# Optimization experiments

Hardware: AMD Instinct MI355X
Metric: run time of the kernel (lower is better)

Reference implementation:

```python
import jax, jax.numpy as jnp
import numpy as np

B, N, DIM, H, DH = 2, 1024, 1024, 8, 64
DI = H * DH  # 512
K = 4        # depthwise conv kernel
EPS = 1.1920929e-07  # float32 eps (torch RMSNorm default)


def setup_inputs() -> dict:
    key = jax.random.key(0)
    ks = jax.random.split(key, 12)
    s = lambda k, shape, sc=0.02: jax.random.normal(k, shape, jnp.float32) * sc
    return dict(
        x=jax.random.normal(ks[0], (B, N, DIM), jnp.float32),
        w_rms=jnp.ones((DIM,), jnp.float32),
        wq=s(ks[1], (DIM, DI)), wk=s(ks[2], (DIM, DI)), wv=s(ks[3], (DIM, DI)),
        wo=s(ks[4], (DI, DIM)),
        conv_q=s(ks[5], (DIM, K), 0.3), conv_k=s(ks[6], (DIM, K), 0.3), conv_v=s(ks[7], (DIM, K), 0.3),
        gamma_q=jnp.ones((H, 1, DH), jnp.float32), gamma_k=jnp.ones((H, 1, DH), jnp.float32),
        lr_w=s(ks[8], (DIM, H)), lr_b=jnp.full((H,), -4.0, jnp.float32),
        decay_w=s(ks[9], (DIM, H)), decay_b=jnp.full((H,), 4.0, jnp.float32),
        mom_w=s(ks[10], (DIM, H)), mom_b=jnp.full((H,), 2.0, jnp.float32),
    )


def rmsnorm(x, w):
    return x * jax.lax.rsqrt(jnp.mean(x * x, -1, keepdims=True) + EPS) * w


def mh_rmsnorm(x, gamma):  # x: (b, h, n, d)
    rms = jnp.sqrt(jnp.sum(x * x, -1, keepdims=True)) * (DH ** -0.5)
    return x / jnp.maximum(rms, 1e-8) * gamma


def dwconv(x, w):  # x: (b, n, dim), w: (dim, K) depthwise, padding K//2 -> length n+1
    y = jax.lax.conv_general_dilated(
        x.transpose(0, 2, 1), w[:, None, :], (1,), [(K // 2, K // 2)],
        feature_group_count=DIM, dimension_numbers=('NCW', 'OIW', 'NCW'))
    return y.transpose(0, 2, 1)


def gated_scan(a, x):  # h_t = a_t h_{t-1} + x_t, h_{-1}=0; a:(bh,t), x:(bh,t,d,d)
    def combine(c1, c2):
        a1, x1 = c1
        a2, x2 = c2
        return a1 * a2, a2 * x1 + x2
    _, h = jax.lax.associative_scan(combine, (a[..., None, None], x), axis=1)
    return h


def reference(x, w_rms, wq, wk, wv, wo, conv_q, conv_k, conv_v,
              gamma_q, gamma_k, lr_w, lr_b, decay_w, decay_b, mom_w, mom_b):
    b, n, _ = x.shape
    xa = rmsnorm(x, w_rms)
    qi, ki, vi = dwconv(xa, conv_q), dwconv(xa, conv_k), dwconv(xa, conv_v)
    split = lambda t: t.reshape(b, -1, H, DH).transpose(0, 2, 1, 3)[:, :, :n]  # (b,h,n,d)
    q = mh_rmsnorm(split(qi @ wq), gamma_q)
    k = mh_rmsnorm(split(ki @ wk), gamma_k)
    v = split(vi @ wv)
    fq = q.reshape(b * H, n, DH)
    fk = k.reshape(b * H, n, DH)
    fv = v.reshape(b * H, n, DH)
    sig = jax.nn.sigmoid
    lr = sig(xa @ lr_w + lr_b).transpose(0, 2, 1).reshape(b * H, n)
    decay = sig(xa @ decay_w + decay_b).transpose(0, 2, 1).reshape(b * H, n)
    mom = sig(xa @ mom_w + mom_b).transpose(0, 2, 1).reshape(b * H, n)
    # S_ref = S0 = 0 (fresh state) => pred = 0, delta_vec = -v
    g = jnp.einsum('bti,btj->btij', -fv, fk)          # (bh, n, d, d)
    Z = gated_scan(mom, g)                             # momentum scan
    S = gated_scan(decay, -lr[..., None, None] * Z)    # memory scan
    S_prev = jnp.concatenate([jnp.zeros_like(S[:, :1]), S[:, :-1]], axis=1)
    y = jnp.einsum('btdp,btp->btd', S_prev, fq)        # retrieval y_t = S_{t-1} psi_t
    y = y.reshape(b, H, n, DH).transpose(0, 2, 1, 3).reshape(b, n, DI)
    return y @ wo
```

## Files before the change

### kernel.cpp

```cpp
#include <hip/hip_runtime.h>
#include <math.h>

#define DEV __device__ __forceinline__

constexpr int Bb   = 2;
constexpr int Seq  = 1024;
constexpr int Dim  = 1024;
constexpr int Hh   = 8;
constexpr int Dh   = 64;
constexpr int Di   = 512;
constexpr int BN   = Bb * Seq;
constexpr int NSEQ = Bb * Hh;
constexpr int CHUNK = 32;
constexpr int CLEN  = Seq / CHUNK;
constexpr float EPSV = 1.1920929e-07f;
constexpr int NT   = 16;

typedef _Float16 half8 __attribute__((ext_vector_type(8)));
typedef float    f32x4 __attribute__((ext_vector_type(4)));

DEV float bf2f(unsigned short u) {
  union { unsigned int i; float f; } x; x.i = ((unsigned int)u) << 16; return x.f;
}
DEV unsigned short f2bf(float f) {
  union { float f; unsigned int i; } x; x.f = f;
  unsigned int r = x.i + 0x7fffu + ((x.i >> 16) & 1u);
  return (unsigned short)(r >> 16);
}
DEV float ldin(const void* p, int f32, size_t i) {
  if (f32) return ((const float*)p)[i];
  return bf2f(((const unsigned short*)p)[i]);
}

struct InPtrs { const void* p[17]; int n[17]; };

__global__ __launch_bounds__(64) void k_sniff(InPtrs ip, int* __restrict__ flags) {
  int b = blockIdx.x, tid = threadIdx.x;
  const unsigned short* u = (const unsigned short*)ip.p[b];
  int count = ip.n[b];
  int j = 2 * tid;
  int valid = 0, bad = 0;
  if (j < count) {
    valid = 1;
    float v = bf2f(u[j]);
    float a = fabsf(v);
    if (!(a >= 1e-12f && a <= 1e4f)) bad = 1;
  }
#pragma unroll
  for (int m = 1; m < 64; m <<= 1) { valid += __shfl_xor(valid, m); bad += __shfl_xor(bad, m); }
  if (tid == 0) flags[b] = (2 * bad > valid) ? 1 : 0;
}

__global__ __launch_bounds__(256) void k_prep_w(
    const void* __restrict__ wq, const void* __restrict__ wk,
    const void* __restrict__ wv, const void* __restrict__ wo,
    const int* __restrict__ flags,
    _Float16* __restrict__ wqT, _Float16* __restrict__ wkT,
    _Float16* __restrict__ wvT, _Float16* __restrict__ woT)
{
  int z = blockIdx.z;
  const void* src = (z == 0) ? wq : ((z == 1) ? wk : ((z == 2) ? wv : wo));
  _Float16* dst   = (z == 0) ? wqT : ((z == 1) ? wkT : ((z == 2) ? wvT : woT));
  int f = flags[(z == 0) ? 2 : ((z == 1) ? 3 : ((z == 2) ? 4 : 5))];
  int Kd = (z < 3) ? Dim : Di;
  int Nn = (z < 3) ? Di : Dim;
  int n0 = blockIdx.x * 64, k0 = blockIdx.y * 64;
  if (n0 >= Nn || k0 >= Kd) return;

  __shared__ float tile[64][65];
  int tid = threadIdx.x;
  int r = tid >> 4, c4 = (tid & 15) * 4;
#pragma unroll
  for (int rr = 0; rr < 4; ++rr) {
    int k = rr * 16 + r;
#pragma unroll
    for (int j = 0; j < 4; ++j)
      tile[k][c4 + j] = ldin(src, f, (size_t)(k0 + k) * Nn + n0 + c4 + j);
  }
  __syncthreads();
#pragma unroll
  for (int rr = 0; rr < 4; ++rr) {
    int n = rr * 16 + r;
    _Float16 o4[4];
#pragma unroll
    for (int j = 0; j < 4; ++j) o4[j] = (_Float16)tile[c4 + j][n];
    *(ushort4*)&dst[(size_t)(n0 + n) * Kd + k0 + c4] = *(ushort4*)o4;
  }
}

__global__ __launch_bounds__(256) void k_prep_gamma(
    const void* __restrict__ gq, const void* __restrict__ gk,
    const void* __restrict__ lr_b, const void* __restrict__ decay_b,
    const void* __restrict__ mom_b,
    const int* __restrict__ flags,
    float* __restrict__ gqf, float* __restrict__ gkf, float* __restrict__ gbf)
{
  int tid = threadIdx.x;
  int f9 = flags[9], f10 = flags[10];
  for (int i = tid; i < Di; i += 256) {
    gqf[i] = ldin(gq, f9, i);
    gkf[i] = ldin(gk, f10, i);
  }
  if (tid < 24) {
    int g = tid >> 3, h = tid & 7;
    const void* Bp = (g == 0) ? lr_b : ((g == 1) ? decay_b : mom_b);
    int fB = (g == 0) ? flags[12] : ((g == 1) ? flags[14] : flags[16]);
    gbf[tid] = ldin(Bp, fB, h);
  }
}

__global__ __launch_bounds__(256) void k_prep_gates(
    const void* __restrict__ lr_w, const void* __restrict__ decay_w,
    const void* __restrict__ mom_w, const int* __restrict__ flags,
    _Float16* __restrict__ WgT)
{
  int row = blockIdx.x;
  int tid = threadIdx.x;
  if (row < 24) {
    int g = row >> 3, h = row & 7;
    const void* W = (g == 0) ? lr_w : ((g == 1) ? decay_w : mom_w);
    int f = (g == 0) ? flags[11] : ((g == 1) ? flags[13] : flags[15]);
#pragma unroll
    for (int it = 0; it < 4; ++it) {
      int d = it * 256 + tid;
      WgT[(size_t)row * Dim + d] = (_Float16)ldin(W, f, (size_t)d * Hh + h);
    }
  } else {
#pragma unroll
    for (int it = 0; it < 4; ++it)
      WgT[(size_t)row * Dim + it * 256 + tid] = (_Float16)0.f;
  }
}

__global__ __launch_bounds__(256) void k_prep_conv(
    const void* __restrict__ cq, const void* __restrict__ ck,
    const void* __restrict__ cv, const int* __restrict__ flags,
    _Float16* __restrict__ wcq, _Float16* __restrict__ wck,
    _Float16* __restrict__ wcv)
{
  int tid = blockIdx.x * 256 + threadIdx.x;
  int f6 = flags[6], f7 = flags[7], f8 = flags[8];
  wcq[tid] = (_Float16)ldin(cq, f6, tid);
  wck[tid] = (_Float16)ldin(ck, f7, tid);
  wcv[tid] = (_Float16)ldin(cv, f8, tid);
}

__global__ __launch_bounds__(256) void k_rms(
    const void* __restrict__ x, const void* __restrict__ w_rms,
    const int* __restrict__ flags, _Float16* __restrict__ xaf)
{
  __shared__ float red[4];
  int r = blockIdx.x;
  int tid = threadIdx.x, lane = tid & 63, wid = tid >> 6;
  int fx = flags[0], fw = flags[1];

  size_t rb = (size_t)r * Dim + tid * 4;
  float v0, v1, v2, v3;
  if (fx) {
    float4 u = *(const float4*)((const float*)x + rb);
    v0 = u.x; v1 = u.y; v2 = u.z; v3 = u.w;
  } else {
    ushort4 u = *(const ushort4*)((const unsigned short*)x + rb);
    v0 = bf2f(u.x); v1 = bf2f(u.y); v2 = bf2f(u.z); v3 = bf2f(u.w);
  }
  float ss = v0 * v0 + v1 * v1 + v2 * v2 + v3 * v3;
#pragma unroll
  for (int m = 1; m < 64; m <<= 1) ss += __shfl_xor(ss, m);
  if (lane == 0) red[wid] = ss;
  __syncthreads();
  float scale = rsqrtf((red[0] + red[1] + red[2] + red[3]) * (1.0f / Dim) + EPSV);

  float w0, w1, w2, w3;
  if (fw) {
    float4 u = *(const float4*)((const float*)w_rms + tid * 4);
    w0 = u.x; w1 = u.y; w2 = u.z; w3 = u.w;
  } else {
    ushort4 u = *(const ushort4*)((const unsigned short*)w_rms + tid * 4);
    w0 = bf2f(u.x); w1 = bf2f(u.y); w2 = bf2f(u.z); w3 = bf2f(u.w);
  }
  _Float16 t4[4] = {(_Float16)(v0 * scale * w0), (_Float16)(v1 * scale * w1),
                    (_Float16)(v2 * scale * w2), (_Float16)(v3 * scale * w3)};
  *(ushort4*)&xaf[rb] = *(ushort4*)t4;
}

__global__ __launch_bounds__(256) void k_gates(
    const _Float16* __restrict__ xaf, const _Float16* __restrict__ WgT,
    const float* __restrict__ gbf,
    float* __restrict__ lr, float* __restrict__ decay, float* __restrict__ mom)
{
  __shared__ __align__(16) _Float16 As[64][40];
  __shared__ __align__(16) _Float16 Bs[64][40];

  int tid = threadIdx.x, lane = tid & 63, wvid = tid >> 6;
  int m0 = blockIdx.x * 64;
  int srow = tid >> 2, scol = (tid & 3) * 8;
  int mrow = lane & 15, quad = lane >> 4;

  f32x4 acc[4];
#pragma unroll
  for (int mi = 0; mi < 4; ++mi) acc[mi] = (f32x4){0.f, 0.f, 0.f, 0.f};

  for (int kt = 0; kt < Dim; kt += 32) {
    __syncthreads();
    *(uint4*)&As[srow][scol] = *(const uint4*)&xaf[(size_t)(m0 + srow) * Dim + kt + scol];
    *(uint4*)&Bs[srow][scol] = *(const uint4*)&WgT[(size_t)srow * Dim + kt + scol];
    __syncthreads();
    half8 bfr = *(const half8*)&Bs[wvid * 16 + mrow][quad * 8];
#pragma unroll
    for (int mi = 0; mi < 4; ++mi) {
      half8 afr = *(const half8*)&As[mi * 16 + mrow][quad * 8];
      acc[mi] = __builtin_amdgcn_mfma_f32_16x16x32_f16(afr, bfr, acc[mi], 0, 0, 0);
    }
  }

  int col = wvid * 16 + mrow;
  if (col < 24) {
    int g = col >> 3, h = col & 7;
    float bias = gbf[col];
    float* Op = (g == 0) ? lr : ((g == 1) ? decay : mom);
#pragma unroll
    for (int mi = 0; mi < 4; ++mi) {
#pragma unroll
      for (int r2 = 0; r2 < 4; ++r2) {
        int row = m0 + mi * 16 + quad * 4 + r2;
        int b = row >> 10, t = row & (Seq - 1);
        float z = acc[mi][r2] + bias;
        Op[(b * Hh + h) * Seq + t] = 1.f / (1.f + expf(-z));
      }
    }
  }
}

__global__ __launch_bounds__(256) void k_conv(
    const _Float16* __restrict__ xaf,
    const _Float16* __restrict__ wcq, const _Float16* __restrict__ wck,
    const _Float16* __restrict__ wcv,
    _Float16* __restrict__ qc, _Float16* __restrict__ kc,
    _Float16* __restrict__ vc)
{
  int tb = blockIdx.x, b = blockIdx.y;
  int t0 = tb * NT;
  int c0 = threadIdx.x * 4;

  _Float16 lwq[16], lwk[16], lwv[16];
  *(uint4*)&lwq[0] = *(const uint4*)&wcq[c0 * 4];
  *(uint4*)&lwq[8] = *(const uint4*)&wcq[c0 * 4 + 8];
  *(uint4*)&lwk[0] = *(const uint4*)&wck[c0 * 4];
  *(uint4*)&lwk[8] = *(const uint4*)&wck[c0 * 4 + 8];
  *(uint4*)&lwv[0] = *(const uint4*)&wcv[c0 * 4];
  *(uint4*)&lwv[8] = *(const uint4*)&wcv[c0 * 4 + 8];

  float win[4][4];
  auto loadrow = [&](int ts, float dst[4]) {
    if (ts >= 0 && ts < Seq) {
      ushort4 u = *(const ushort4*)&xaf[((size_t)(b * Seq + ts)) * Dim + c0];
      _Float16 hx[4]; *(ushort4*)hx = u;
      dst[0] = (float)hx[0]; dst[1] = (float)hx[1];
      dst[2] = (float)hx[2]; dst[3] = (float)hx[3];
    } else {
      dst[0] = 0.f; dst[1] = 0.f; dst[2] = 0.f; dst[3] = 0.f;
    }
  };
  loadrow(t0 - 2, win[0]);
  loadrow(t0 - 1, win[1]);
  loadrow(t0,     win[2]);

#pragma unroll
  for (int tt = 0; tt < NT; ++tt) {
    int t = t0 + tt;
    loadrow(t + 1, win[(tt + 3) & 3]);
    const float* r0 = win[(tt + 0) & 3];
    const float* r1 = win[(tt + 1) & 3];
    const float* r2 = win[(tt + 2) & 3];
    const float* r3 = win[(tt + 3) & 3];

    _Float16 tq[4], tk[4], tv[4];
#pragma unroll
    for (int j = 0; j < 4; ++j) {
      float aq = r0[j] * (float)lwq[j * 4 + 0] + r1[j] * (float)lwq[j * 4 + 1]
               + r2[j] * (float)lwq[j * 4 + 2] + r3[j] * (float)lwq[j * 4 + 3];
      float ak = r0[j] * (float)lwk[j * 4 + 0] + r1[j] * (float)lwk[j * 4 + 1]
               + r2[j] * (float)lwk[j * 4 + 2] + r3[j] * (float)lwk[j * 4 + 3];
      float av = r0[j] * (float)lwv[j * 4 + 0] + r1[j] * (float)lwv[j * 4 + 1]
               + r2[j] * (float)lwv[j * 4 + 2] + r3[j] * (float)lwv[j * 4 + 3];
      tq[j] = (_Float16)aq; tk[j] = (_Float16)ak; tv[j] = (_Float16)av;
    }
    size_t o = ((size_t)(b * Seq + t)) * Dim + c0;
    *(ushort4*)&qc[o] = *(ushort4*)tq;
    *(ushort4*)&kc[o] = *(ushort4*)tk;
    *(ushort4*)&vc[o] = *(ushort4*)tv;
  }
}

__global__ __launch_bounds__(256) void k_gemm_bt(
    const _Float16* __restrict__ A0, const _Float16* __restrict__ A1,
    const _Float16* __restrict__ A2,
    const _Float16* __restrict__ B0, const _Float16* __restrict__ B1,
    const _Float16* __restrict__ B2,
    void* __restrict__ C0, void* __restrict__ C1, void* __restrict__ C2,
    const int* __restrict__ flags,
    int Nn, int Kd, int is_final)
{
  int z = blockIdx.z;
  const _Float16* A  = (z == 0) ? A0 : ((z == 1) ? A1 : A2);
  const _Float16* Bt = (z == 0) ? B0 : ((z == 1) ? B1 : B2);
  void* C = (z == 0) ? C0 : ((z == 1) ? C1 : C2);

  __shared__ __align__(16) _Float16 As[64][40];
  __shared__ __align__(16) _Float16 Bs[64][40];

  int tid = threadIdx.x, lane = tid & 63, wvid = tid >> 6;
  int n0 = blockIdx.x * 64, m0 = blockIdx.y * 64;
  int srow = tid >> 2, scol = (tid & 3) * 8;
  int mrow = lane & 15, quad = lane >> 4;

  f32x4 acc[4];
#pragma unroll
  for (int mi = 0; mi < 4; ++mi) acc[mi] = (f32x4){0.f, 0.f, 0.f, 0.f};

  for (int kt = 0; kt < Kd; kt += 32) {
    __syncthreads();
    *(uint4*)&As[srow][scol] = *(const uint4*)&A[(size_t)(m0 + srow) * Kd + kt + scol];
    *(uint4*)&Bs[srow][scol] = *(const uint4*)&Bt[(size_t)(n0 + srow) * Kd + kt + scol];
    __syncthreads();
    half8 bfr = *(const half8*)&Bs[wvid * 16 + mrow][quad * 8];
#pragma unroll
    for (int mi = 0; mi < 4; ++mi) {
      half8 afr = *(const half8*)&As[mi * 16 + mrow][quad * 8];
      acc[mi] = __builtin_amdgcn_mfma_f32_16x16x32_f16(afr, bfr, acc[mi], 0, 0, 0);
    }
  }

  int any_bf16 = 0;
  if (is_final) {
#pragma unroll
    for (int i2 = 0; i2 < 17; ++i2) any_bf16 |= (flags[i2] == 0);
  }

  int col = n0 + wvid * 16 + mrow;
#pragma unroll
  for (int mi = 0; mi < 4; ++mi) {
#pragma unroll
    for (int r2 = 0; r2 < 4; ++r2) {
      int row = m0 + mi * 16 + quad * 4 + r2;
      float v = acc[mi][r2];
      size_t idx = (size_t)row * Nn + col;
      if (!is_final)        ((_Float16*)C)[idx] = (_Float16)v;
      else if (any_bf16)    ((unsigned short*)C)[idx] = f2bf(v);
      else                  ((float*)C)[idx] = v;
    }
  }
}

__global__ __launch_bounds__(256) void k_phaseA(
    const _Float16* __restrict__ kpre, const _Float16* __restrict__ vpre,
    const float* __restrict__ gkf,
    const float* __restrict__ lr, const float* __restrict__ decay,
    const float* __restrict__ mom,
    _Float16* __restrict__ ZS_Z, _Float16* __restrict__ ZS_S,
    float* __restrict__ Mc, float* __restrict__ Dc, float* __restrict__ Wc)
{
  int c = blockIdx.x, s = blockIdx.y;
  int b = s >> 3, h = s & 7;
  int tid = threadIdx.x, lane = tid & 63, wv = tid >> 6;
  int i = tid >> 2, j0 = (tid & 3) * 16;
  __shared__ float kn[CLEN][64], vv[CLEN][64];
  __shared__ float gl[CLEN], gd[CLEN], gm[CLEN];

  {
    int t = tid >> 3, col = (tid & 7) * 8;
    size_t g = ((size_t)(b * Seq + c * CLEN + t)) * Di + h * 64 + col;
    half8 kv = *(const half8*)&kpre[g];
    half8 vvv = *(const half8*)&vpre[g];
#pragma unroll
    for (int j = 0; j < 8; ++j) { kn[t][col + j] = (float)kv[j]; vv[t][col + j] = (float)vvv[j]; }
    if (tid < 96) {
      int which = tid >> 5, t2 = tid & 31;
      const float* gp = (which == 0) ? lr : ((which == 1) ? decay : mom);
      float val = gp[s * Seq + c * CLEN + t2];
      if (which == 0) gl[t2] = val; else if (which == 1) gd[t2] = val; else gm[t2] = val;
    }
  }
  __syncthreads();
  {
    float gk = gkf[h * 64 + lane];
#pragma unroll
    for (int tt = 0; tt < 8; ++tt) {
      int t = wv * 8 + tt;
      float kvv = kn[t][lane];
      float ss = kvv * kvv;
#pragma unroll
      for (int m = 1; m < 64; m <<= 1) ss += __shfl_xor(ss, m);
      kn[t][lane] = kvv * (1.f / fmaxf(sqrtf(ss) * 0.125f, 1e-8f)) * gk;
    }
  }
  __syncthreads();

  float Zl[16], Sl[16];
#pragma unroll
  for (int jj = 0; jj < 16; ++jj) { Zl[jj] = 0.f; Sl[jj] = 0.f; }
  float Mcum = 1.f, Dcum = 1.f, wacc = 0.f;

  for (int t = 0; t < CLEN; ++t) {
    float l = gl[t], dd = gd[t], mm = gm[t];
    float vi = vv[t][i];
    Mcum *= mm;
#pragma unroll
    for (int jj = 0; jj < 16; ++jj) {
      Zl[jj] = fmaf(mm, Zl[jj], -vi * kn[t][j0 + jj]);
      Sl[jj] = fmaf(dd, Sl[jj], -l * Zl[jj]);
    }
    wacc = fmaf(dd, wacc, -l * Mcum);
    Dcum *= dd;
  }
  size_t base = ((size_t)(s * CHUNK + c)) * 4096 + (size_t)i * 64 + j0;
  half8 zo0, zo1, so0, so1;
#pragma unroll
  for (int jj = 0; jj < 8; ++jj) {
    zo0[jj] = (_Float16)Zl[jj];     zo1[jj] = (_Float16)Zl[jj + 8];
    so0[jj] = (_Float16)Sl[jj];     so1[jj] = (_Float16)Sl[jj + 8];
  }
  *(half8*)&ZS_Z[base] = zo0; *(half8*)&ZS_Z[base + 8] = zo1;
  *(half8*)&ZS_S[base] = so0; *(half8*)&ZS_S[base + 8] = so1;
  if (tid == 0) {
    Mc[s * CHUNK + c] = Mcum; Dc[s * CHUNK + c] = Dcum; Wc[s * CHUNK + c] = wacc;
  }
}

__global__ __launch_bounds__(256) void k_phaseB(
    _Float16* __restrict__ ZS_Z, _Float16* __restrict__ ZS_S,
    const float* __restrict__ Mc, const float* __restrict__ Dc,
    const float* __restrict__ Wc)
{
  int s = blockIdx.x;
  int e = blockIdx.y * 256 + threadIdx.x;
  float Z = 0.f, S = 0.f;
  for (int c = 0; c < CHUNK; ++c) {
    size_t base = ((size_t)(s * CHUNK + c)) * 4096 + e;
    float mc = Mc[s * CHUNK + c], dc = Dc[s * CHUNK + c], wc = Wc[s * CHUNK + c];
    float zl = (float)ZS_Z[base], sl = (float)ZS_S[base];
    ZS_Z[base] = (_Float16)Z; ZS_S[base] = (_Float16)S;
    S = fmaf(dc, S, fmaf(wc, Z, sl));
    Z = fmaf(mc, Z, zl);
  }
}

__global__ __launch_bounds__(256) void k_phaseC(
    const _Float16* __restrict__ qpre, const _Float16* __restrict__ kpre,
    const _Float16* __restrict__ vpre,
    const float* __restrict__ gqf, const float* __restrict__ gkf,
    const float* __restrict__ lr, const float* __restrict__ decay,
    const float* __restrict__ mom,
    const _Float16* __restrict__ ZS_Z, const _Float16* __restrict__ ZS_S,
    _Float16* __restrict__ yb)
{
  int c = blockIdx.x, s = blockIdx.y;
  int b = s >> 3, h = s & 7;
  int tid = threadIdx.x, lane = tid & 63, wv = tid >> 6;
  int i = tid >> 2, j0 = (tid & 3) * 16;
  __shared__ float kn[CLEN][64], vv[CLEN][64], qn[CLEN][64];
  __shared__ float gl[CLEN], gd[CLEN], gm[CLEN];

  float Zi_[16], Si_[16], Zl[16], Sl[16];
  size_t base = ((size_t)(s * CHUNK + c)) * 4096 + (size_t)i * 64 + j0;
  {
    half8 z0 = *(const half8*)&ZS_Z[base], z1 = *(const half8*)&ZS_Z[base + 8];
    half8 s0 = *(const half8*)&ZS_S[base], s1 = *(const half8*)&ZS_S[base + 8];
#pragma unroll
    for (int jj = 0; jj < 8; ++jj) {
      Zi_[jj] = (float)z0[jj]; Zi_[jj + 8] = (float)z1[jj];
      Si_[jj] = (float)s0[jj]; Si_[jj + 8] = (float)s1[jj];
      Zl[jj] = 0.f; Zl[jj + 8] = 0.f; Sl[jj] = 0.f; Sl[jj + 8] = 0.f;
    }
  }
  {
    int t = tid >> 3, col = (tid & 7) * 8;
    size_t g = ((size_t)(b * Seq + c * CLEN + t)) * Di + h * 64 + col;
    half8 kv = *(const half8*)&kpre[g];
    half8 vvv = *(const half8*)&vpre[g];
    half8 qv = *(const half8*)&qpre[g];
#pragma unroll
    for (int j = 0; j < 8; ++j) {
      kn[t][col + j] = (float)kv[j]; vv[t][col + j] = (float)vvv[j];
      qn[t][col + j] = (float)qv[j];
    }
    if (tid < 96) {
      int which = tid >> 5, t2 = tid & 31;
      const float* gp = (which == 0) ? lr : ((which == 1) ? decay : mom);
      float val = gp[s * Seq + c * CLEN + t2];
      if (which == 0) gl[t2] = val; else if (which == 1) gd[t2] = val; else gm[t2] = val;
    }
  }
  __syncthreads();
  {
    float gk = gkf[h * 64 + lane];
    float gq = gqf[h * 64 + lane];
#pragma unroll
    for (int tt = 0; tt < 8; ++tt) {
      int t = wv * 8 + tt;
      float kvv = kn[t][lane];
      float ssk = kvv * kvv;
      float qvv = qn[t][lane];
      float ssq = qvv * qvv;
#pragma unroll
      for (int m = 1; m < 64; m <<= 1) { ssk += __shfl_xor(ssk, m); ssq += __shfl_xor(ssq, m); }
      kn[t][lane] = kvv * (1.f / fmaxf(sqrtf(ssk) * 0.125f, 1e-8f)) * gk;
      qn[t][lane] = qvv * (1.f / fmaxf(sqrtf(ssq) * 0.125f, 1e-8f)) * gq;
    }
  }
  __syncthreads();

  float Mcum = 1.f, Dcum = 1.f, wacc = 0.f;
  float Dprev = 1.f, wprev = 0.f;

  for (int t = 0; t < CLEN; ++t) {
    float l = gl[t], dd = gd[t], mm = gm[t];

    float yp = 0.f;
#pragma unroll
    for (int jj = 0; jj < 16; ++jj) {
      float tmp = fmaf(Dprev, Si_[jj], fmaf(wprev, Zi_[jj], Sl[jj]));
      yp = fmaf(tmp, qn[t][j0 + jj], yp);
    }
    yp += __shfl_xor(yp, 1);
    yp += __shfl_xor(yp, 2);
    if ((tid & 3) == 0)
      yb[((size_t)(b * Seq + c * CLEN + t)) * Di + h * 64 + i] = (_Float16)yp;

    float vi = vv[t][i];
    Mcum *= mm;
#pragma unroll
    for (int jj = 0; jj < 16; ++jj) {
      Zl[jj] = fmaf(mm, Zl[jj], -vi * kn[t][j0 + jj]);
      Sl[jj] = fmaf(dd, Sl[jj], -l * Zl[jj]);
    }
    wacc = fmaf(dd, wacc, -l * Mcum);
    Dcum *= dd;
    Dprev = Dcum; wprev = wacc;
  }
}

extern "C" void kernel_launch(void* const* d_in, const int* in_sizes, int n_in,
                              void* d_out, int out_size, void* d_ws, size_t ws_size,
                              hipStream_t stream) {
  InPtrs ip;
  for (int i = 0; i < 17; ++i) { ip.p[i] = d_in[i]; ip.n[i] = in_sizes[i]; }

  char* p = (char*)d_ws;
  auto take = [&](size_t bytes) -> char* {
    char* q = p; p += (bytes + 255) & ~(size_t)255; return q;
  };
  int* flags           = (int*)take(32 * 4);
  _Float16* xaf        = (_Float16*)take((size_t)BN * Dim * 2);
  _Float16* qc         = (_Float16*)take((size_t)BN * Dim * 2);
  _Float16* kc         = (_Float16*)take((size_t)BN * Dim * 2);
  _Float16* vc         = (_Float16*)take((size_t)BN * Dim * 2);
  _Float16* qpre       = (_Float16*)take((size_t)BN * Di * 2);
  _Float16* kpre       = (_Float16*)take((size_t)BN * Di * 2);
  _Float16* vpre       = (_Float16*)take((size_t)BN * Di * 2);
  float* lrA           = (float*)take((size_t)NSEQ * Seq * 4);
  float* decayA        = (float*)take((size_t)NSEQ * Seq * 4);
  float* momA          = (float*)take((size_t)NSEQ * Seq * 4);
  float* Mc            = (float*)take((size_t)NSEQ * CHUNK * 4);
  float* Dc            = (float*)take((size_t)NSEQ * CHUNK * 4);
  float* Wc            = (float*)take((size_t)NSEQ * CHUNK * 4);
  _Float16* wqT        = (_Float16*)take((size_t)Di * Dim * 2);
  _Float16* wkT        = (_Float16*)take((size_t)Di * Dim * 2);
  _Float16* wvT        = (_Float16*)take((size_t)Di * Dim * 2);
  _Float16* woT        = (_Float16*)take((size_t)Dim * Di * 2);
  _Float16* WgT        = (_Float16*)take((size_t)64 * Dim * 2);
  _Float16* wcq        = (_Float16*)take((size_t)Dim * 4 * 2);
  _Float16* wck        = (_Float16*)take((size_t)Dim * 4 * 2);
  _Float16* wcv        = (_Float16*)take((size_t)Dim * 4 * 2);
  float* gqf           = (float*)take(Di * 4);
  float* gkf           = (float*)take(Di * 4);
  float* gbf           = (float*)take(32 * 4);
  _Float16* ZS_Z       = qc;
  _Float16* ZS_S       = kc;
  _Float16* yb         = vc;

  k_sniff<<<17, 64, 0, stream>>>(ip, flags);
  k_prep_w<<<dim3(16, 16, 4), 256, 0, stream>>>(d_in[2], d_in[3], d_in[4], d_in[5],
                                                flags, wqT, wkT, wvT, woT);
  k_prep_gamma<<<1, 256, 0, stream>>>(d_in[9], d_in[10], d_in[12], d_in[14], d_in[16],
                                      flags, gqf, gkf, gbf);
  k_prep_gates<<<64, 256, 0, stream>>>(d_in[11], d_in[13], d_in[15], flags, WgT);
  k_prep_conv<<<16, 256, 0, stream>>>(d_in[6], d_in[7], d_in[8], flags, wcq, wck, wcv);

  k_rms<<<BN, 256, 0, stream>>>(d_in[0], d_in[1], flags, xaf);
  k_gates<<<BN / 64, 256, 0, stream>>>(xaf, WgT, gbf, lrA, decayA, momA);
  k_conv<<<dim3(Seq / NT, Bb), 256, 0, stream>>>(xaf, wcq, wck, wcv, qc, kc, vc);

  dim3 g1(Di / 64, BN / 64, 3);
  k_gemm_bt<<<g1, 256, 0, stream>>>(qc, kc, vc, wqT, wkT, wvT,
                                    qpre, kpre, vpre, flags, Di, Dim, 0);

  k_phaseA<<<dim3(CHUNK, NSEQ), 256, 0, stream>>>(kpre, vpre, gkf,
                                                  lrA, decayA, momA,
                                                  ZS_Z, ZS_S, Mc, Dc, Wc);
  k_phaseB<<<dim3(NSEQ, 16), 256, 0, stream>>>(ZS_Z, ZS_S, Mc, Dc, Wc);
  k_phaseC<<<dim3(CHUNK, NSEQ), 256, 0, stream>>>(qpre, kpre, vpre, gqf, gkf,
                                                  lrA, decayA, momA,
                                                  ZS_Z, ZS_S, yb);

  dim3 g2(Dim / 64, BN / 64, 1);
  k_gemm_bt<<<g2, 256, 0, stream>>>(yb, yb, yb, woT, woT, woT,
                                    d_out, d_out, d_out, flags, Dim, Di, 1);
}
```

Before: 211.2 us.

## Merge weight-prep kernels into one launch and enlarge GEMM tiles to 128x64

Four small preprocessing kernels (weight transpose, gate weights, conv weights, gamma/bias) are merged into one launch that dispatches on block index, removing three launch overheads. The GEMM grows its M tile from 64 to 128, and each wave now computes a 32x64 sub-tile with four B fragments reused across two A fragments. This gives more MFMA work per shared-memory load. In exchange the grid has half as many blocks, which may lower occupancy on the QKV and output projections, and each thread holds more accumulator registers.

Measured after the change: 208.4 us. No clear change (-1.3%).

```diff
diff --git a/kernel.cpp b/kernel.cpp
--- a/kernel.cpp
+++ b/kernel.cpp
@@ -51,98 +51,90 @@
   if (tid == 0) flags[b] = (2 * bad > valid) ? 1 : 0;
 }
 
-__global__ __launch_bounds__(256) void k_prep_w(
+__global__ __launch_bounds__(256) void k_prep_all(
     const void* __restrict__ wq, const void* __restrict__ wk,
     const void* __restrict__ wv, const void* __restrict__ wo,
-    const int* __restrict__ flags,
-    _Float16* __restrict__ wqT, _Float16* __restrict__ wkT,
-    _Float16* __restrict__ wvT, _Float16* __restrict__ woT)
-{
-  int z = blockIdx.z;
-  const void* src = (z == 0) ? wq : ((z == 1) ? wk : ((z == 2) ? wv : wo));
-  _Float16* dst   = (z == 0) ? wqT : ((z == 1) ? wkT : ((z == 2) ? wvT : woT));
-  int f = flags[(z == 0) ? 2 : ((z == 1) ? 3 : ((z == 2) ? 4 : 5))];
-  int Kd = (z < 3) ? Dim : Di;
-  int Nn = (z < 3) ? Di : Dim;
-  int n0 = blockIdx.x * 64, k0 = blockIdx.y * 64;
-  if (n0 >= Nn || k0 >= Kd) return;
-
-  __shared__ float tile[64][65];
-  int tid = threadIdx.x;
-  int r = tid >> 4, c4 = (tid & 15) * 4;
-#pragma unroll
-  for (int rr = 0; rr < 4; ++rr) {
-    int k = rr * 16 + r;
-#pragma unroll
-    for (int j = 0; j < 4; ++j)
-      tile[k][c4 + j] = ldin(src, f, (size_t)(k0 + k) * Nn + n0 + c4 + j);
-  }
-  __syncthreads();
-#pragma unroll
-  for (int rr = 0; rr < 4; ++rr) {
-    int n = rr * 16 + r;
-    _Float16 o4[4];
-#pragma unroll
-    for (int j = 0; j < 4; ++j) o4[j] = (_Float16)tile[c4 + j][n];
-    *(ushort4*)&dst[(size_t)(n0 + n) * Kd + k0 + c4] = *(ushort4*)o4;
-  }
-}
-
-__global__ __launch_bounds__(256) void k_prep_gamma(
+    const void* __restrict__ lr_w, const void* __restrict__ decay_w,
+    const void* __restrict__ mom_w,
+    const void* __restrict__ cq, const void* __restrict__ ck,
+    const void* __restrict__ cv,
     const void* __restrict__ gq, const void* __restrict__ gk,
     const void* __restrict__ lr_b, const void* __restrict__ decay_b,
     const void* __restrict__ mom_b,
     const int* __restrict__ flags,
+    _Float16* __restrict__ wqT, _Float16* __restrict__ wkT,
+    _Float16* __restrict__ wvT, _Float16* __restrict__ woT,
+    _Float16* __restrict__ WgT,
+    _Float16* __restrict__ wcq, _Float16* __restrict__ wck,
+    _Float16* __restrict__ wcv,
     float* __restrict__ gqf, float* __restrict__ gkf, float* __restrict__ gbf)
 {
+  int blk = blockIdx.x;
   int tid = threadIdx.x;
-  int f9 = flags[9], f10 = flags[10];
-  for (int i = tid; i < Di; i += 256) {
-    gqf[i] = ldin(gq, f9, i);
-    gkf[i] = ldin(gk, f10, i);
-  }
-  if (tid < 24) {
-    int g = tid >> 3, h = tid & 7;
-    const void* Bp = (g == 0) ? lr_b : ((g == 1) ? decay_b : mom_b);
-    int fB = (g == 0) ? flags[12] : ((g == 1) ? flags[14] : flags[16]);
-    gbf[tid] = ldin(Bp, fB, h);
-  }
-}
-
-__global__ __launch_bounds__(256) void k_prep_gates(
-    const void* __restrict__ lr_w, const void* __restrict__ decay_w,
-    const void* __restrict__ mom_w, const int* __restrict__ flags,
-    _Float16* __restrict__ WgT)
-{
-  int row = blockIdx.x;
-  int tid = threadIdx.x;
-  if (row < 24) {
-    int g = row >> 3, h = row & 7;
-    const void* W = (g == 0) ? lr_w : ((g == 1) ? decay_w : mom_w);
-    int f = (g == 0) ? flags[11] : ((g == 1) ? flags[13] : flags[15]);
-#pragma unroll
-    for (int it = 0; it < 4; ++it) {
-      int d = it * 256 + tid;
-      WgT[(size_t)row * Dim + d] = (_Float16)ldin(W, f, (size_t)d * Hh + h);
-    }
+
+  if (blk < 1024) {
+    int z = blk >> 8, bx = blk & 15, by = (blk >> 4) & 15;
+    const void* src = (z == 0) ? wq : ((z == 1) ? wk : ((z == 2) ? wv : wo));
+    _Float16* dst   = (z == 0) ? wqT : ((z == 1) ? wkT : ((z == 2) ? wvT : woT));
+    int f = flags[(z == 0) ? 2 : ((z == 1) ? 3 : ((z == 2) ? 4 : 5))];
+    int Kd = (z < 3) ? Dim : Di;
+    int Nn = (z < 3) ? Di : Dim;
+    int n0 = bx * 64, k0 = by * 64;
+    if (n0 >= Nn || k0 >= Kd) return;
+
+    __shared__ float tile[64][65];
+    int r = tid >> 4, c4 = (tid & 15) * 4;
+#pragma unroll
+    for (int rr = 0; rr < 4; ++rr) {
+      int k = rr * 16 + r;
+#pragma unroll
+      for (int j = 0; j < 4; ++j)
+        tile[k][c4 + j] = ldin(src, f, (size_t)(k0 + k) * Nn + n0 + c4 + j);
+    }
+    __syncthreads();
+#pragma unroll
+    for (int rr = 0; rr < 4; ++rr) {
+      int n = rr * 16 + r;
+      _Float16 o4[4];
+#pragma unroll
+      for (int j = 0; j < 4; ++j) o4[j] = (_Float16)tile[c4 + j][n];
+      *(ushort4*)&dst[(size_t)(n0 + n) * Kd + k0 + c4] = *(ushort4*)o4;
+    }
+  } else if (blk < 1088) {
+    int row = blk - 1024;
+    if (row < 24) {
+      int g = row >> 3, h = row & 7;
+      const void* W = (g == 0) ? lr_w : ((g == 1) ? decay_w : mom_w);
+      int f = (g == 0) ? flags[11] : ((g == 1) ? flags[13] : flags[15]);
+#pragma unroll
+      for (int it = 0; it < 4; ++it) {
+        int d = it * 256 + tid;
+        WgT[(size_t)row * Dim + d] = (_Float16)ldin(W, f, (size_t)d * Hh + h);
+      }
+    } else {
+#pragma unroll
+      for (int it = 0; it < 4; ++it)
+        WgT[(size_t)row * Dim + it * 256 + tid] = (_Float16)0.f;
+    }
+  } else if (blk < 1104) {
+    int e = (blk - 1088) * 256 + tid;
+    int f6 = flags[6], f7 = flags[7], f8 = flags[8];
+    wcq[e] = (_Float16)ldin(cq, f6, e);
+    wck[e] = (_Float16)ldin(ck, f7, e);
+    wcv[e] = (_Float16)ldin(cv, f8, e);
   } else {
-#pragma unroll
-    for (int it = 0; it < 4; ++it)
-      WgT[(size_t)row * Dim + it * 256 + tid] = (_Float16)0.f;
-  }
-}
-
-__global__ __launch_bounds__(256) void k_prep_conv(
-    const void* __restrict__ cq, const void* __restrict__ ck,
-    const void* __restrict__ cv, const int* __restrict__ flags,
-    _Float16* __restrict__ wcq, _Float16* __restrict__ wck,
-    _Float16* __restrict__ wcv)
-{
-  int tid = blockIdx.x * 256 + threadIdx.x;
-  int f6 = flags[6], f7 = flags[7], f8 = flags[8];
-  wcq[tid] = (_Float16)ldin(cq, f6, tid);
-  wck[tid] = (_Float16)ldin(ck, f7, tid);
-  wcv[tid] = (_Float16)ldin(cv, f8, tid);
+    int f9 = flags[9], f10 = flags[10];
+    for (int i = tid; i < Di; i += 256) {
+      gqf[i] = ldin(gq, f9, i);
+      gkf[i] = ldin(gk, f10, i);
+    }
+    if (tid < 24) {
+      int g = tid >> 3, h = tid & 7;
+      const void* Bp = (g == 0) ? lr_b : ((g == 1) ? decay_b : mom_b);
+      int fB = (g == 0) ? flags[12] : ((g == 1) ? flags[14] : flags[16]);
+      gbf[tid] = ldin(Bp, fB, h);
+    }
+  }
 }
 
 __global__ __launch_bounds__(256) void k_rms(
@@ -292,7 +284,7 @@
   }
 }
 
-__global__ __launch_bounds__(256) void k_gemm_bt(
+__global__ __launch_bounds__(256) void k_gemm_128(
     const _Float16* __restrict__ A0, const _Float16* __restrict__ A1,
     const _Float16* __restrict__ A2,
     const _Float16* __restrict__ B0, const _Float16* __restrict__ B1,
@@ -306,28 +298,40 @@
   const _Float16* Bt = (z == 0) ? B0 : ((z == 1) ? B1 : B2);
   void* C = (z == 0) ? C0 : ((z == 1) ? C1 : C2);
 
-  __shared__ __align__(16) _Float16 As[64][40];
+  __shared__ __align__(16) _Float16 As[128][40];
   __shared__ __align__(16) _Float16 Bs[64][40];
 
-  int tid = threadIdx.x, lane = tid & 63, wvid = tid >> 6;
-  int n0 = blockIdx.x * 64, m0 = blockIdx.y * 64;
-  int srow = tid >> 2, scol = (tid & 3) * 8;
+  int tid = threadIdx.x, lane = tid & 63, wv = tid >> 6;
+  int n0 = blockIdx.x * 64, m0 = blockIdx.y * 128;
   int mrow = lane & 15, quad = lane >> 4;
-
-  f32x4 acc[4];
-#pragma unroll
-  for (int mi = 0; mi < 4; ++mi) acc[mi] = (f32x4){0.f, 0.f, 0.f, 0.f};
+  int wm = wv * 32;
+
+  int ar0 = tid >> 2,        ac0 = (tid & 3) * 8;
+  int ar1 = (tid + 256) >> 2;
+
+  f32x4 acc[2][4];
+#pragma unroll
+  for (int mi = 0; mi < 2; ++mi)
+#pragma unroll
+    for (int ni = 0; ni < 4; ++ni) acc[mi][ni] = (f32x4){0.f, 0.f, 0.f, 0.f};
 
   for (int kt = 0; kt < Kd; kt += 32) {
     __syncthreads();
-    *(uint4*)&As[srow][scol] = *(const uint4*)&A[(size_t)(m0 + srow) * Kd + kt + scol];
-    *(uint4*)&Bs[srow][scol] = *(const uint4*)&Bt[(size_t)(n0 + srow) * Kd + kt + scol];
+    *(uint4*)&As[ar0][ac0] = *(const uint4*)&A[(size_t)(m0 + ar0) * Kd + kt + ac0];
+    *(uint4*)&As[ar1][ac0] = *(const uint4*)&A[(size_t)(m0 + ar1) * Kd + kt + ac0];
+    *(uint4*)&Bs[ar0][ac0] = *(const uint4*)&Bt[(size_t)(n0 + ar0) * Kd + kt + ac0];
     __syncthreads();
-    half8 bfr = *(const half8*)&Bs[wvid * 16 + mrow][quad * 8];
-#pragma unroll
-    for (int mi = 0; mi < 4; ++mi) {
-      half8 afr = *(const half8*)&As[mi * 16 + mrow][quad * 8];
-      acc[mi] = __builtin_amdgcn_mfma_f32_16x16x32_f16(afr, bfr, acc[mi], 0, 0, 0);
+
+    half8 bfr[4];
+#pragma unroll
+    for (int ni = 0; ni < 4; ++ni)
+      bfr[ni] = *(const half8*)&Bs[ni * 16 + mrow][quad * 8];
+#pragma unroll
+    for (int mi = 0; mi < 2; ++mi) {
+      half8 afr = *(const half8*)&As[wm + mi * 16 + mrow][quad * 8];
+#pragma unroll
+      for (int ni = 0; ni < 4; ++ni)
+        acc[mi][ni] = __builtin_amdgcn_mfma_f32_16x16x32_f16(afr, bfr[ni], acc[mi][ni], 0, 0, 0);
     }
   }
 
@@ -337,17 +341,20 @@
     for (int i2 = 0; i2 < 17; ++i2) any_bf16 |= (flags[i2] == 0);
   }
 
-  int col = n0 + wvid * 16 + mrow;
-#pragma unroll
-  for (int mi = 0; mi < 4; ++mi) {
-#pragma unroll
-    for (int r2 = 0; r2 < 4; ++r2) {
-      int row = m0 + mi * 16 + quad * 4 + r2;
-      float v = acc[mi][r2];
-      size_t idx = (size_t)row * Nn + col;
-      if (!is_final)        ((_Float16*)C)[idx] = (_Float16)v;
-      else if (any_bf16)    ((unsigned short*)C)[idx] = f2bf(v);
-      else                  ((float*)C)[idx] = v;
+#pragma unroll
+  for (int mi = 0; mi < 2; ++mi) {
+#pragma unroll
+    for (int ni = 0; ni < 4; ++ni) {
+      int col = n0 + ni * 16 + mrow;
+#pragma unroll
+      for (int r2 = 0; r2 < 4; ++r2) {
+        int row = m0 + wm + mi * 16 + quad * 4 + r2;
+        float v = acc[mi][ni][r2];
+        size_t idx = (size_t)row * Nn + col;
+        if (!is_final)        ((_Float16*)C)[idx] = (_Float16)v;
+        else if (any_bf16)    ((unsigned short*)C)[idx] = f2bf(v);
+        else                  ((float*)C)[idx] = v;
+      }
     }
   }
 }
@@ -580,20 +587,20 @@
   _Float16* yb         = vc;
 
   k_sniff<<<17, 64, 0, stream>>>(ip, flags);
-  k_prep_w<<<dim3(16, 16, 4), 256, 0, stream>>>(d_in[2], d_in[3], d_in[4], d_in[5],
-                                                flags, wqT, wkT, wvT, woT);
-  k_prep_gamma<<<1, 256, 0, stream>>>(d_in[9], d_in[10], d_in[12], d_in[14], d_in[16],
-                                      flags, gqf, gkf, gbf);
-  k_prep_gates<<<64, 256, 0, stream>>>(d_in[11], d_in[13], d_in[15], flags, WgT);
-  k_prep_conv<<<16, 256, 0, stream>>>(d_in[6], d_in[7], d_in[8], flags, wcq, wck, wcv);
+  k_prep_all<<<1105, 256, 0, stream>>>(
+      d_in[2], d_in[3], d_in[4], d_in[5],
+      d_in[11], d_in[13], d_in[15],
+      d_in[6], d_in[7], d_in[8],
+      d_in[9], d_in[10], d_in[12], d_in[14], d_in[16],
+      flags, wqT, wkT, wvT, woT, WgT, wcq, wck, wcv, gqf, gkf, gbf);
 
   k_rms<<<BN, 256, 0, stream>>>(d_in[0], d_in[1], flags, xaf);
   k_gates<<<BN / 64, 256, 0, stream>>>(xaf, WgT, gbf, lrA, decayA, momA);
   k_conv<<<dim3(Seq / NT, Bb), 256, 0, stream>>>(xaf, wcq, wck, wcv, qc, kc, vc);
 
-  dim3 g1(Di / 64, BN / 64, 3);
-  k_gemm_bt<<<g1, 256, 0, stream>>>(qc, kc, vc, wqT, wkT, wvT,
-                                    qpre, kpre, vpre, flags, Di, Dim, 0);
+  dim3 g1(Di / 64, BN / 128, 3);
+  k_gemm_128<<<g1, 256, 0, stream>>>(qc, kc, vc, wqT, wkT, wvT,
+                                     qpre, kpre, vpre, flags, Di, Dim, 0);
 
   k_phaseA<<<dim3(CHUNK, NSEQ), 256, 0, stream>>>(kpre, vpre, gkf,
                                                   lrA, decayA, momA,
@@ -603,7 +610,7 @@
                                                   lrA, decayA, momA,
                                                   ZS_Z, ZS_S, yb);
 
-  dim3 g2(Dim / 64, BN / 64, 1);
-  k_gemm_bt<<<g2, 256, 0, stream>>>(yb, yb, yb, woT, woT, woT,
-                                    d_out, d_out, d_out, flags, Dim, Di, 1);
-}
+  dim3 g2(Dim / 64, BN / 128, 1);
+  k_gemm_128<<<g2, 256, 0, stream>>>(yb, yb, yb, woT, woT, woT,
+                                     d_out, d_out, d_out, flags, Dim, Di, 1);
+}
```
